# Kernel tuning notes

Measured on AMD Instinct MI355X. Metric: run time of the kernel, lower is better.

Reference implementation:

```python
import jax, jax.numpy as jnp
import numpy as np
from jax import lax

DN = ('NCHW', 'OIHW', 'NCHW')

def conv2d(x, w, b, stride, pad):
    y = lax.conv_general_dilated(x, w, (stride, stride), [(pad, pad), (pad, pad)], dimension_numbers=DN)
    return y + b[None, :, None, None]

def conv_transpose2d(x, w, b):
    # torch ConvTranspose2d(k=4, s=2, p=1): weight is (in, out, kH, kW).
    # Equivalent dilated conv: flip spatial dims, swap in/out, lhs_dilation=2, pad=k-1-p=2.
    kernel = jnp.flip(w, (2, 3)).transpose(1, 0, 2, 3)  # (out, in, 4, 4)
    y = lax.conv_general_dilated(x, kernel, (1, 1), [(2, 2), (2, 2)], lhs_dilation=(2, 2), dimension_numbers=DN)
    return y + b[None, :, None, None]

def res_block(x, w, b):
    return x + jax.nn.relu(conv2d(x, w, b, 1, 1))

def setup_inputs() -> dict:
    key = jax.random.key(0)
    ks = jax.random.split(key, 20)
    F_, K, D = 16, 64, 16  # num_features, num_embeddings, embedding_dim
    s = 0.05
    inp = {
        'x': jax.random.normal(ks[0], (64, 1, 256, 256), jnp.float32),
        'conv1_w': jax.random.normal(ks[1], (F_, 1, 4, 4), jnp.float32) * s,
        'conv1_b': jnp.zeros((F_,), jnp.float32),
        'conv2_w': jax.random.normal(ks[2], (F_, F_, 4, 4), jnp.float32) * s,
        'conv2_b': jnp.zeros((F_,), jnp.float32),
        'er1_w': jax.random.normal(ks[3], (F_, F_, 3, 3), jnp.float32) * s,
        'er1_b': jnp.zeros((F_,), jnp.float32),
        'er2_w': jax.random.normal(ks[4], (F_, F_, 3, 3), jnp.float32) * s,
        'er2_b': jnp.zeros((F_,), jnp.float32),
        'codebook': jax.random.normal(ks[5], (K, D), jnp.float32),
        'dr1_w': jax.random.normal(ks[6], (F_, F_, 3, 3), jnp.float32) * s,
        'dr1_b': jnp.zeros((F_,), jnp.float32),
        'dr2_w': jax.random.normal(ks[7], (F_, F_, 3, 3), jnp.float32) * s,
        'dr2_b': jnp.zeros((F_,), jnp.float32),
        'tc1_w': jax.random.normal(ks[8], (F_, F_, 4, 4), jnp.float32) * s,  # ConvTranspose (in,out,kH,kW)
        'tc1_b': jnp.zeros((F_,), jnp.float32),
        'tc2_w': jax.random.normal(ks[9], (F_, 1, 4, 4), jnp.float32) * s,
        'tc2_b': jnp.zeros((1,), jnp.float32),
    }
    return inp

def reference(x, conv1_w, conv1_b, conv2_w, conv2_b, er1_w, er1_b, er2_w, er2_b,
              codebook, dr1_w, dr1_b, dr2_w, dr2_b, tc1_w, tc1_b, tc2_w, tc2_b):
    # Encoder
    h = jax.nn.relu(conv2d(x, conv1_w, conv1_b, 2, 1))
    h = jax.nn.relu(conv2d(h, conv2_w, conv2_b, 2, 1))
    h = res_block(h, er1_w, er1_b)
    h = res_block(h, er2_w, er2_b)  # (B, 16, 64, 64)
    # VQ: faithful to torch's encoded.view(-1, C) raw NCHW flatten
    C = h.shape[1]
    flat = h.reshape(-1, C)  # (N, 16)
    # squared L2 distances without materializing (N, K, D) broadcast tensor
    d = (jnp.sum(flat * flat, axis=1, keepdims=True)
         - 2.0 * flat @ codebook.T
         + jnp.sum(codebook * codebook, axis=1)[None, :])  # (N, K)
    indices = jnp.argmin(d, axis=1)  # (N,)
    quantized = codebook[indices].reshape(h.shape)
    # Decoder
    q = res_block(quantized, dr1_w, dr1_b)
    q = res_block(q, dr2_w, dr2_b)
    q = jax.nn.relu(conv_transpose2d(q, tc1_w, tc1_b))
    decoded = conv_transpose2d(q, tc2_w, tc2_b)  # (B, 1, 256, 256)
    return decoded, indices
```

## Files before the change

### kernel.cpp

```cpp
#include <hip/hip_runtime.h>
#include <hip/hip_bf16.h>


#define R8X(M)  M(0) M(1) M(2) M(3) M(4) M(5) M(6) M(7)

typedef __attribute__((ext_vector_type(8))) short          bf16x8;
typedef __attribute__((ext_vector_type(8))) unsigned short u16x8;
typedef __attribute__((ext_vector_type(4))) float          f32x4;

__device__ __forceinline__ unsigned short f2bf(float f) {
    unsigned u; __builtin_memcpy(&u, &f, 4);
    unsigned r = u + 0x7FFFu + ((u >> 16) & 1u);
    return (unsigned short)(r >> 16);
}
__device__ __forceinline__ float bf2f(unsigned short h) {
    unsigned u = ((unsigned)h) << 16;
    float f; __builtin_memcpy(&f, &u, 4);
    return f;
}

__global__ __launch_bounds__(256) void conv1_k(const float* __restrict__ x, const float* __restrict__ w,
                                               const float* __restrict__ bias,
                                               unsigned short* __restrict__ oh, unsigned short* __restrict__ ol) {
    int idx = blockIdx.x * 256 + threadIdx.x;
    int ox = idx & 127;
    int oy = (idx >> 7) & 127;
    int b  = idx >> 14;
    const float* xin = x + (size_t)b * 65536;
    float pv[16];
#pragma unroll
    for (int ky = 0; ky < 4; ++ky) {
        int iy = 2 * oy - 1 + ky;
#pragma unroll
        for (int kx = 0; kx < 4; ++kx) {
            int ix = 2 * ox - 1 + kx;
            pv[ky * 4 + kx] = (iy >= 0 && iy < 256 && ix >= 0 && ix < 256)
                                  ? xin[iy * 256 + ix] : 0.f;
        }
    }
    u16x8 h0, h1, l0, l1;
#pragma unroll
    for (int oc = 0; oc < 16; ++oc) {
        float acc = bias[oc];
#pragma unroll
        for (int k = 0; k < 16; ++k) acc = fmaf(pv[k], w[oc * 16 + k], acc);
        float r = fmaxf(acc, 0.f);
        unsigned short hb = f2bf(r);
        unsigned short lb = f2bf(r - bf2f(hb));
        if (oc < 8) { h0[oc] = hb; l0[oc] = lb; }
        else        { h1[oc - 8] = hb; l1[oc - 8] = lb; }
    }
    u16x8* po = (u16x8*)(oh + (size_t)idx * 16);
    po[0] = h0; po[1] = h1;
    u16x8* pl = (u16x8*)(ol + (size_t)idx * 16);
    pl[0] = l0; pl[1] = l1;
}

__global__ __launch_bounds__(256) void conv2_mfma_k(const unsigned short* __restrict__ fh,
                                                    const unsigned short* __restrict__ fl,
                                                    const float* __restrict__ w, const float* __restrict__ bias,
                                                    float* __restrict__ out) {
    __shared__ unsigned short wsh[16 * 264];
    __shared__ unsigned short wsl[16 * 264];
    for (int i = threadIdx.x; i < 4096; i += 256) {
        int oc = i >> 8, k = i & 255;
        int ic = k & 15, tap = k >> 4;
        float f = w[oc * 256 + ic * 16 + tap];
        unsigned short hb = f2bf(f);
        wsh[oc * 264 + k] = hb;
        wsl[oc * 264 + k] = f2bf(f - bf2f(hb));
    }
    __syncthreads();

    int wid  = threadIdx.x >> 6;
    int lane = threadIdx.x & 63;
    int col = lane & 15;
    int kg  = lane >> 4;
    int ic0 = (kg & 1) * 8;
    float accb = bias[col];
    int gw = blockIdx.x * 4 + wid;

    for (int t = 0; t < 2; ++t) {
        int tile = gw * 2 + t;
        int v0  = (tile & 3) * 16;
        int y   = (tile >> 2) & 63;
        int img = tile >> 8;
        const unsigned short* bh = fh + (size_t)img * 262144;
        const unsigned short* bl = fl + (size_t)img * 262144;
        f32x4 acc = { accb, accb, accb, accb };
#pragma unroll
        for (int m = 0; m < 8; ++m) {
            int tap = 2 * m + (kg >> 1);
            int ty = tap >> 2, tx = tap & 3;
            int jy = 2 * y - 1 + ty;
            int jx = 2 * (v0 + col) - 1 + tx;
            bf16x8 ah = { 0, 0, 0, 0, 0, 0, 0, 0 };
            bf16x8 al = { 0, 0, 0, 0, 0, 0, 0, 0 };
            if (jy >= 0 && jy < 128 && jx >= 0 && jx < 128) {
                size_t off = ((size_t)(jy * 128 + jx)) * 16 + ic0;
                ah = *(const bf16x8*)(bh + off);
                al = *(const bf16x8*)(bl + off);
            }
            bf16x8 wh = *(const bf16x8*)&wsh[col * 264 + m * 32 + kg * 8];
            bf16x8 wl = *(const bf16x8*)&wsl[col * 264 + m * 32 + kg * 8];
            acc = __builtin_amdgcn_mfma_f32_16x16x32_bf16(ah, wh, acc, 0, 0, 0);
            acc = __builtin_amdgcn_mfma_f32_16x16x32_bf16(al, wh, acc, 0, 0, 0);
            acc = __builtin_amdgcn_mfma_f32_16x16x32_bf16(ah, wl, acc, 0, 0, 0);
        }
        float* o = out + (size_t)img * 65536 + col * 4096 + y * 64 + v0;
#pragma unroll
        for (int r = 0; r < 4; ++r) {
            int px = kg * 4 + r;
            o[px] = fmaxf(acc[r], 0.f);
        }
    }
}

__global__ __launch_bounds__(256) void res_k(const float* __restrict__ in, const float* __restrict__ w,
                                             const float* __restrict__ bias, float* __restrict__ out) {
    int half = blockIdx.x >> 10;
    int idx  = (blockIdx.x & 1023) * 256 + threadIdx.x;
    int ox = idx & 63;
    int oy = (idx >> 6) & 63;
    int b  = idx >> 12;
    int ocb = half * 8;
    const float* xin = in + (size_t)b * 65536;
    const float* wb  = w + (size_t)ocb * 144;
#define DECLB(i) float a##i = bias[ocb + i];
    R8X(DECLB)
#undef DECLB
    bool yt = (oy > 0), yb = (oy < 63);
    bool xl = (ox > 0), xr = (ox < 63);
    for (int ic = 0; ic < 16; ++ic) {
        const float* xb = xin + ic * 4096 + (oy - 1) * 64 + (ox - 1);
        float pa0 = (yt && xl) ? xb[0]       : 0.f;
        float pa1 =  yt        ? xb[1]       : 0.f;
        float pa2 = (yt && xr) ? xb[2]       : 0.f;
        float pb0 =  xl        ? xb[64 + 0]  : 0.f;
        float pb1 =              xb[64 + 1];
        float pb2 =  xr        ? xb[64 + 2]  : 0.f;
        float pc0 = (yb && xl) ? xb[128 + 0] : 0.f;
        float pc1 =  yb        ? xb[128 + 1] : 0.f;
        float pc2 = (yb && xr) ? xb[128 + 2] : 0.f;
        const float* wp = wb + ic * 9;
#define FMAR(oc) { const float* q = wp + oc * 144; \
        a##oc = fmaf(pa0, q[0], a##oc); a##oc = fmaf(pa1, q[1], a##oc); a##oc = fmaf(pa2, q[2], a##oc); \
        a##oc = fmaf(pb0, q[3], a##oc); a##oc = fmaf(pb1, q[4], a##oc); a##oc = fmaf(pb2, q[5], a##oc); \
        a##oc = fmaf(pc0, q[6], a##oc); a##oc = fmaf(pc1, q[7], a##oc); a##oc = fmaf(pc2, q[8], a##oc); }
        R8X(FMAR)
#undef FMAR
    }
    float* o        = out + (size_t)b * 65536 + (size_t)ocb * 4096 + oy * 64 + ox;
    const float* rr = xin + (size_t)ocb * 4096 + oy * 64 + ox;
#define RSTO(oc) o[oc * 4096] = rr[oc * 4096] + fmaxf(a##oc, 0.f);
    R8X(RSTO)
#undef RSTO
}

__global__ __launch_bounds__(256) void vq_k(const float* __restrict__ h, const float* __restrict__ cb,
                                            unsigned short* __restrict__ q, float* __restrict__ idx_out) {
    __shared__ float cbs[1024];
    __shared__ float cn[64];
    for (int i = threadIdx.x; i < 1024; i += 256) cbs[i] = cb[i];
    __syncthreads();
    if (threadIdx.x < 64) {
        float s = 0.f;
#pragma unroll
        for (int d = 0; d < 16; ++d) { float v = cbs[threadIdx.x * 16 + d]; s = fmaf(v, v, s); }
        cn[threadIdx.x] = s;
    }
    __syncthreads();
    int r = blockIdx.x * 256 + threadIdx.x;
    float f[16];
    const float4* hp = (const float4*)(h + (size_t)r * 16);
#pragma unroll
    for (int j = 0; j < 4; ++j) {
        float4 v = hp[j];
        f[j * 4 + 0] = v.x; f[j * 4 + 1] = v.y; f[j * 4 + 2] = v.z; f[j * 4 + 3] = v.w;
    }
    float best = 3.4e38f;
    int bi = 0;
    for (int k = 0; k < 64; ++k) {
        float dot = 0.f;
#pragma unroll
        for (int d = 0; d < 16; ++d) dot = fmaf(f[d], cbs[k * 16 + d], dot);
        float dist = cn[k] - 2.f * dot;
        if (dist < best) { best = dist; bi = k; }
    }
    u16x8 q0, q1;
#pragma unroll
    for (int d = 0; d < 8; ++d) {
        q0[d] = f2bf(cbs[bi * 16 + d]);
        q1[d] = f2bf(cbs[bi * 16 + 8 + d]);
    }
    u16x8* qp = (u16x8*)(q + (size_t)r * 16);
    qp[0] = q0; qp[1] = q1;
    idx_out[r] = (float)bi;
}

__global__ __launch_bounds__(256) void trans_k(const unsigned short* __restrict__ in,
                                               unsigned short* __restrict__ out) {
    __shared__ unsigned short lds[16 * 64];
    int b = blockIdx.x >> 6;
    int y = blockIdx.x & 63;
    int t = threadIdx.x;
    {
        int c = t >> 4, x0 = (t & 15) * 4;
        const unsigned short* p = in + (((size_t)(b * 16 + c) * 64 + y) << 6) + x0;
#pragma unroll
        for (int j = 0; j < 4; ++j) lds[c * 64 + x0 + j] = p[j];
    }
    __syncthreads();
    {
        int xx = t >> 2, c0 = (t & 3) * 4;
        unsigned short* p = out + (((size_t)(b * 64 + y) * 64 + xx) << 4) + c0;
#pragma unroll
        for (int j = 0; j < 4; ++j) p[j] = lds[(c0 + j) * 64 + xx];
    }
}

__global__ __launch_bounds__(256) void res_mfma_k(const unsigned short* __restrict__ in,
                                                  const float* __restrict__ w, const float* __restrict__ bias,
                                                  unsigned short* __restrict__ outb) {
    int wid  = threadIdx.x >> 6;
    int lane = threadIdx.x & 63;
    int col = lane & 15;
    int kg  = lane >> 4;
    int ic0 = (kg & 1) * 8;

    bf16x8 bw[5];
#pragma unroll
    for (int m = 0; m < 5; ++m) {
        int tap = 2 * m + (kg >> 1);
        bf16x8 t = { 0, 0, 0, 0, 0, 0, 0, 0 };
        if (tap < 9) {
#pragma unroll
            for (int j = 0; j < 8; ++j)
                t[j] = (short)f2bf(w[(col * 16 + ic0 + j) * 9 + tap]);
        }
        bw[m] = t;
    }
    float accb = bias[col];

    int gw = blockIdx.x * 4 + wid;
    for (int t = 0; t < 8; ++t) {
        int tile = gw * 8 + t;
        int v0  = (tile & 3) * 16;
        int y   = (tile >> 2) & 63;
        int img = tile >> 8;
        const unsigned short* xi = in + (size_t)img * 65536;
        f32x4 acc = { accb, accb, accb, accb };
#pragma unroll
        for (int m = 0; m < 5; ++m) {
            int tap = 2 * m + (kg >> 1);
            bf16x8 a = { 0, 0, 0, 0, 0, 0, 0, 0 };
            if (tap < 9) {
                int ty = tap / 3, tx = tap - ty * 3;
                int jy = y + ty - 1;
                int jx = v0 + col + tx - 1;
                if (jy >= 0 && jy < 64 && jx >= 0 && jx < 64)
                    a = *(const bf16x8*)(xi + ((jy * 64 + jx) * 16 + ic0));
            }
            acc = __builtin_amdgcn_mfma_f32_16x16x32_bf16(a, bw[m], acc, 0, 0, 0);
        }
#pragma unroll
        for (int r = 0; r < 4; ++r) {
            int px = v0 + kg * 4 + r;
            size_t ad = (size_t)(y * 64 + px) * 16 + col;
            float vin = bf2f(xi[ad]);
            outb[(size_t)img * 65536 + ad] = f2bf(vin + fmaxf(acc[r], 0.f));
        }
    }
}

__global__ __launch_bounds__(256) void tconv1_mfma_k(const unsigned short* __restrict__ xb,
                                                     const float* __restrict__ w1, const float* __restrict__ bia,
                                                     unsigned short* __restrict__ outb) {
    int cls = blockIdx.x >> 9;
    int bb  = blockIdx.x & 511;
    int DY = cls >> 1, DX = cls & 1;
    int wid  = threadIdx.x >> 6;
    int lane = threadIdx.x & 63;
    int oc = lane & 15;
    int kg = lane >> 4;

    bf16x8 bfr0, bfr1;
    float accb = bia[oc];
#pragma unroll
    for (int m = 0; m < 2; ++m) {
        int tap = 2 * m + (kg >> 1);
        int ty = tap >> 1, tx = tap & 1;
        int koff = (3 - DY - 2 * ty) * 4 + (3 - DX - 2 * tx);
        int ic0 = (kg & 1) * 8;
        bf16x8 t;
#pragma unroll
        for (int j = 0; j < 8; ++j)
            t[j] = (short)f2bf(w1[(ic0 + j) * 256 + oc * 16 + koff]);
        if (m == 0) bfr0 = t; else bfr1 = t;
    }

    int Wc = bb * 4 + wid;
    for (int t = 0; t < 8; ++t) {
        int tile = Wc * 8 + t;
        int v0  = (tile & 3) * 16;
        int u   = (tile >> 2) & 63;
        int img = tile >> 8;
        const unsigned short* xi = xb + (size_t)img * 65536;
        f32x4 acc = { accb, accb, accb, accb };
#pragma unroll
        for (int m = 0; m < 2; ++m) {
            int tap = 2 * m + (kg >> 1);
            int ty = tap >> 1, tx = tap & 1;
            int jy = u + DY - 1 + ty;
            int jx = v0 + oc + DX - 1 + tx;
            bf16x8 a = { 0, 0, 0, 0, 0, 0, 0, 0 };
            if (jy >= 0 && jy < 64 && jx >= 0 && jx < 64) {
                int ic0 = (kg & 1) * 8;
                a = *(const bf16x8*)(xi + ((jy * 64 + jx) * 16 + ic0));
            }
            acc = __builtin_amdgcn_mfma_f32_16x16x32_bf16(a, (m == 0 ? bfr0 : bfr1), acc, 0, 0, 0);
        }
        int my = 2 * u + DY;
#pragma unroll
        for (int r = 0; r < 4; ++r) {
            int pxr = kg * 4 + r;
            int mx  = 2 * (v0 + pxr) + DX;
            outb[(((size_t)img * 16384) + my * 128 + mx) * 16 + oc] = f2bf(fmaxf(acc[r], 0.f));
        }
    }
}

template <int RY, int RX>
__device__ __forceinline__ void quad_contrib(const unsigned short* __restrict__ px,
                                             const float* __restrict__ w2,
                                             float& a00, float& a01, float& a10, float& a11) {
    constexpr int nY = (RY == 0) ? 2 : 1;
    constexpr int nX = (RX == 0) ? 2 : 1;
    constexpr int dyA[2] = { (RY == 1) ? 1 : 0, 1 };
    constexpr int kyA[2] = { (RY == -1) ? 3 : ((RY == 0) ? 1 : 0), 2 };
    constexpr int dxA[2] = { (RX == 1) ? 1 : 0, 1 };
    constexpr int kxA[2] = { (RX == -1) ? 3 : ((RX == 0) ? 1 : 0), 2 };
    u16x8 h0 = *(const u16x8*)px;
    u16x8 h1 = *(const u16x8*)(px + 8);
#pragma unroll
    for (int iy = 0; iy < nY; ++iy) {
#pragma unroll
        for (int ix = 0; ix < nX; ++ix) {
            const int ky = kyA[iy], kx = kxA[ix];
            float& a = (dyA[iy] == 0) ? ((dxA[ix] == 0) ? a00 : a01)
                                      : ((dxA[ix] == 0) ? a10 : a11);
#pragma unroll
            for (int ic = 0; ic < 8; ++ic)
                a = fmaf(bf2f(h0[ic]), w2[ic * 16 + ky * 4 + kx], a);
#pragma unroll
            for (int ic = 0; ic < 8; ++ic)
                a = fmaf(bf2f(h1[ic]), w2[(ic + 8) * 16 + ky * 4 + kx], a);
        }
    }
}

__global__ __launch_bounds__(256) void tconv2_quad_k(const unsigned short* __restrict__ f1b,
                                                     const float* __restrict__ w2, const float* __restrict__ b2,
                                                     float* __restrict__ out) {
    int idx = blockIdx.x * 256 + threadIdx.x;
    int v = idx & 127;
    int u = (idx >> 7) & 127;
    int b = idx >> 14;
    const unsigned short* fb = f1b + (size_t)b * 262144;
    float b2s = b2[0];
    float a00 = b2s, a01 = b2s, a10 = b2s, a11 = b2s;

#define QC(RY, RX) { int jy = u + (RY), jx = v + (RX); \
    if (jy >= 0 && jy < 128 && jx >= 0 && jx < 128) \
        quad_contrib<RY, RX>(fb + ((size_t)(jy * 128 + jx) << 4), w2, a00, a01, a10, a11); }
    QC(-1, -1) QC(-1, 0) QC(-1, 1)
    QC( 0, -1) QC( 0, 0) QC( 0, 1)
    QC( 1, -1) QC( 1, 0) QC( 1, 1)
#undef QC

    float* o = out + (size_t)b * 65536 + (2 * u) * 256 + 2 * v;
    float2 r0; r0.x = a00; r0.y = a01;
    float2 r1; r1.x = a10; r1.y = a11;
    *(float2*)o         = r0;
    *(float2*)(o + 256) = r1;
}

extern "C" void kernel_launch(void* const* d_in, const int* in_sizes, int n_in,
                              void* d_out, int out_size, void* d_ws, size_t ws_size,
                              hipStream_t stream) {
    const float* x    = (const float*)d_in[0];
    const float* c1w  = (const float*)d_in[1];
    const float* c1b  = (const float*)d_in[2];
    const float* c2w  = (const float*)d_in[3];
    const float* c2b  = (const float*)d_in[4];
    const float* er1w = (const float*)d_in[5];
    const float* er1b = (const float*)d_in[6];
    const float* er2w = (const float*)d_in[7];
    const float* er2b = (const float*)d_in[8];
    const float* cb   = (const float*)d_in[9];
    const float* dr1w = (const float*)d_in[10];
    const float* dr1b = (const float*)d_in[11];
    const float* dr2w = (const float*)d_in[12];
    const float* dr2b = (const float*)d_in[13];
    const float* t1w  = (const float*)d_in[14];
    const float* t1b  = (const float*)d_in[15];
    const float* t2w  = (const float*)d_in[16];
    const float* t2b  = (const float*)d_in[17];

    char* W = (char*)d_ws;
    const size_t MB = 1024 * 1024;
    unsigned short* f1h   = (unsigned short*)(W + 0);
    unsigned short* f1l   = (unsigned short*)(W + 32 * MB);
    float*          f2c   = (float*)         (W + 64 * MB);
    float*          fer1  = (float*)         (W + 80 * MB);
    float*          fer2  = (float*)         (W + 96 * MB);
    unsigned short* qn    = (unsigned short*)(W + 112 * MB);
    unsigned short* qc    = (unsigned short*)(W + 128 * MB);
    unsigned short* d1o   = (unsigned short*)(W + 144 * MB);
    unsigned short* d2o   = (unsigned short*)(W + 160 * MB);
    unsigned short* t1o   = (unsigned short*)(W + 176 * MB);

    float* out     = (float*)d_out;
    float* idx_out = out + 4194304;

    conv1_k      <<<4096, 256, 0, stream>>>(x, c1w, c1b, f1h, f1l);
    conv2_mfma_k <<<2048, 256, 0, stream>>>(f1h, f1l, c2w, c2b, f2c);
    res_k        <<<2048, 256, 0, stream>>>(f2c, er1w, er1b, fer1);
    res_k        <<<2048, 256, 0, stream>>>(fer1, er2w, er2b, fer2);
    vq_k         <<<1024, 256, 0, stream>>>(fer2, cb, qn, idx_out);
    trans_k      <<<4096, 256, 0, stream>>>(qn, qc);
    res_mfma_k   <<< 512, 256, 0, stream>>>(qc, dr1w, dr1b, d1o);
    res_mfma_k   <<< 512, 256, 0, stream>>>(d1o, dr2w, dr2b, d2o);
    tconv1_mfma_k<<<2048, 256, 0, stream>>>(d2o, t1w, t1b, t1o);
    tconv2_quad_k<<<4096, 256, 0, stream>>>(t1o, t2w, t2b, out);
}
```

Before: 223.4 us.

## Move encoder residual convs to split-bf16 MFMA with NHWC hi/lo activations

Replaces the scalar FP32 encoder residual-block kernel with an MFMA kernel that uses a split-bf16 (hi+lo) three-product scheme to keep near-FP32 accuracy. conv2 now writes its output as NHWC hi/lo bf16 pairs, so the first residual block reads them directly and writes hi/lo again. The second block writes NCHW float for the VQ stage. This cuts the scalar FMA work and the float memory traffic of the two encoder res blocks, at the cost of less scattered-store efficiency and some bf16 split precision.

```diff
diff --git a/kernel.cpp b/kernel.cpp
--- a/kernel.cpp
+++ b/kernel.cpp
@@ -59,7 +59,7 @@
 __global__ __launch_bounds__(256) void conv2_mfma_k(const unsigned short* __restrict__ fh,
                                                     const unsigned short* __restrict__ fl,
                                                     const float* __restrict__ w, const float* __restrict__ bias,
-                                                    float* __restrict__ out) {
+                                                    unsigned short* __restrict__ oh, unsigned short* __restrict__ ol) {
     __shared__ unsigned short wsh[16 * 264];
     __shared__ unsigned short wsl[16 * 264];
     for (int i = threadIdx.x; i < 4096; i += 256) {
@@ -107,54 +107,87 @@
             acc = __builtin_amdgcn_mfma_f32_16x16x32_bf16(al, wh, acc, 0, 0, 0);
             acc = __builtin_amdgcn_mfma_f32_16x16x32_bf16(ah, wl, acc, 0, 0, 0);
         }
-        float* o = out + (size_t)img * 65536 + col * 4096 + y * 64 + v0;
 #pragma unroll
         for (int r = 0; r < 4; ++r) {
-            int px = kg * 4 + r;
-            o[px] = fmaxf(acc[r], 0.f);
-        }
-    }
-}
-
-__global__ __launch_bounds__(256) void res_k(const float* __restrict__ in, const float* __restrict__ w,
-                                             const float* __restrict__ bias, float* __restrict__ out) {
-    int half = blockIdx.x >> 10;
-    int idx  = (blockIdx.x & 1023) * 256 + threadIdx.x;
-    int ox = idx & 63;
-    int oy = (idx >> 6) & 63;
-    int b  = idx >> 12;
-    int ocb = half * 8;
-    const float* xin = in + (size_t)b * 65536;
-    const float* wb  = w + (size_t)ocb * 144;
-#define DECLB(i) float a##i = bias[ocb + i];
-    R8X(DECLB)
-#undef DECLB
-    bool yt = (oy > 0), yb = (oy < 63);
-    bool xl = (ox > 0), xr = (ox < 63);
-    for (int ic = 0; ic < 16; ++ic) {
-        const float* xb = xin + ic * 4096 + (oy - 1) * 64 + (ox - 1);
-        float pa0 = (yt && xl) ? xb[0]       : 0.f;
-        float pa1 =  yt        ? xb[1]       : 0.f;
-        float pa2 = (yt && xr) ? xb[2]       : 0.f;
-        float pb0 =  xl        ? xb[64 + 0]  : 0.f;
-        float pb1 =              xb[64 + 1];
-        float pb2 =  xr        ? xb[64 + 2]  : 0.f;
-        float pc0 = (yb && xl) ? xb[128 + 0] : 0.f;
-        float pc1 =  yb        ? xb[128 + 1] : 0.f;
-        float pc2 = (yb && xr) ? xb[128 + 2] : 0.f;
-        const float* wp = wb + ic * 9;
-#define FMAR(oc) { const float* q = wp + oc * 144; \
-        a##oc = fmaf(pa0, q[0], a##oc); a##oc = fmaf(pa1, q[1], a##oc); a##oc = fmaf(pa2, q[2], a##oc); \
-        a##oc = fmaf(pb0, q[3], a##oc); a##oc = fmaf(pb1, q[4], a##oc); a##oc = fmaf(pb2, q[5], a##oc); \
-        a##oc = fmaf(pc0, q[6], a##oc); a##oc = fmaf(pc1, q[7], a##oc); a##oc = fmaf(pc2, q[8], a##oc); }
-        R8X(FMAR)
-#undef FMAR
-    }
-    float* o        = out + (size_t)b * 65536 + (size_t)ocb * 4096 + oy * 64 + ox;
-    const float* rr = xin + (size_t)ocb * 4096 + oy * 64 + ox;
-#define RSTO(oc) o[oc * 4096] = rr[oc * 4096] + fmaxf(a##oc, 0.f);
-    R8X(RSTO)
-#undef RSTO
+            int xx = v0 + kg * 4 + r;
+            size_t ad = (size_t)img * 65536 + ((size_t)(y * 64 + xx)) * 16 + col;
+            float rv = fmaxf(acc[r], 0.f);
+            unsigned short hb = f2bf(rv);
+            oh[ad] = hb;
+            ol[ad] = f2bf(rv - bf2f(hb));
+        }
+    }
+}
+
+template <int OUTMODE>
+__global__ __launch_bounds__(256) void er_mfma_k(const unsigned short* __restrict__ inh,
+                                                 const unsigned short* __restrict__ inl,
+                                                 const float* __restrict__ w, const float* __restrict__ bias,
+                                                 unsigned short* __restrict__ oh, unsigned short* __restrict__ ol,
+                                                 float* __restrict__ ofp) {
+    __shared__ unsigned short wsh[16 * 176];
+    __shared__ unsigned short wsl[16 * 176];
+    for (int i = threadIdx.x; i < 2816; i += 256) {
+        int oc = i / 176, k = i % 176;
+        float f = (k < 144) ? w[(oc * 16 + (k & 15)) * 9 + (k >> 4)] : 0.f;
+        unsigned short hb = f2bf(f);
+        wsh[i] = hb;
+        wsl[i] = f2bf(f - bf2f(hb));
+    }
+    __syncthreads();
+
+    int wid  = threadIdx.x >> 6;
+    int lane = threadIdx.x & 63;
+    int col = lane & 15;
+    int kg  = lane >> 4;
+    int ic0 = (kg & 1) * 8;
+    float accb = bias[col];
+    int gw = blockIdx.x * 4 + wid;
+
+    for (int t = 0; t < 8; ++t) {
+        int tile = gw * 8 + t;
+        int v0  = (tile & 3) * 16;
+        int y   = (tile >> 2) & 63;
+        int img = tile >> 8;
+        const unsigned short* xh = inh + (size_t)img * 65536;
+        const unsigned short* xl = inl + (size_t)img * 65536;
+        f32x4 acc = { accb, accb, accb, accb };
+#pragma unroll
+        for (int m = 0; m < 5; ++m) {
+            int tap = 2 * m + (kg >> 1);
+            bf16x8 ah = { 0, 0, 0, 0, 0, 0, 0, 0 };
+            bf16x8 al = { 0, 0, 0, 0, 0, 0, 0, 0 };
+            if (tap < 9) {
+                int ty = tap / 3, tx = tap - ty * 3;
+                int jy = y + ty - 1;
+                int jx = v0 + col + tx - 1;
+                if (jy >= 0 && jy < 64 && jx >= 0 && jx < 64) {
+                    size_t off = ((size_t)(jy * 64 + jx)) * 16 + ic0;
+                    ah = *(const bf16x8*)(xh + off);
+                    al = *(const bf16x8*)(xl + off);
+                }
+            }
+            bf16x8 wh = *(const bf16x8*)&wsh[col * 176 + m * 32 + kg * 8];
+            bf16x8 wl = *(const bf16x8*)&wsl[col * 176 + m * 32 + kg * 8];
+            acc = __builtin_amdgcn_mfma_f32_16x16x32_bf16(ah, wh, acc, 0, 0, 0);
+            acc = __builtin_amdgcn_mfma_f32_16x16x32_bf16(al, wh, acc, 0, 0, 0);
+            acc = __builtin_amdgcn_mfma_f32_16x16x32_bf16(ah, wl, acc, 0, 0, 0);
+        }
+#pragma unroll
+        for (int r = 0; r < 4; ++r) {
+            int px = v0 + kg * 4 + r;
+            size_t ad = ((size_t)(y * 64 + px)) * 16 + col;
+            float vin = bf2f(xh[ad]) + bf2f(xl[ad]);
+            float res = vin + fmaxf(acc[r], 0.f);
+            if (OUTMODE == 0) {
+                unsigned short hb = f2bf(res);
+                oh[(size_t)img * 65536 + ad] = hb;
+                ol[(size_t)img * 65536 + ad] = f2bf(res - bf2f(hb));
+            } else {
+                ofp[(size_t)img * 65536 + (size_t)col * 4096 + y * 64 + px] = res;
+            }
+        }
+    }
 }
 
 __global__ __launch_bounds__(256) void vq_k(const float* __restrict__ h, const float* __restrict__ cb,
@@ -409,25 +442,27 @@
 
     char* W = (char*)d_ws;
     const size_t MB = 1024 * 1024;
-    unsigned short* f1h   = (unsigned short*)(W + 0);
-    unsigned short* f1l   = (unsigned short*)(W + 32 * MB);
-    float*          f2c   = (float*)         (W + 64 * MB);
-    float*          fer1  = (float*)         (W + 80 * MB);
-    float*          fer2  = (float*)         (W + 96 * MB);
-    unsigned short* qn    = (unsigned short*)(W + 112 * MB);
-    unsigned short* qc    = (unsigned short*)(W + 128 * MB);
-    unsigned short* d1o   = (unsigned short*)(W + 144 * MB);
-    unsigned short* d2o   = (unsigned short*)(W + 160 * MB);
-    unsigned short* t1o   = (unsigned short*)(W + 176 * MB);
+    unsigned short* f1h = (unsigned short*)(W + 0);
+    unsigned short* f1l = (unsigned short*)(W + 32 * MB);
+    unsigned short* c2h = (unsigned short*)(W + 64 * MB);
+    unsigned short* c2l = (unsigned short*)(W + 80 * MB);
+    unsigned short* e1h = (unsigned short*)(W + 96 * MB);
+    unsigned short* e1l = (unsigned short*)(W + 112 * MB);
+    float*          e2f = (float*)         (W + 128 * MB);
+    unsigned short* qn  = (unsigned short*)(W + 152 * MB);
+    unsigned short* qc  = (unsigned short*)(W + 168 * MB);
+    unsigned short* d1o = (unsigned short*)(W + 184 * MB);
+    unsigned short* d2o = (unsigned short*)(W + 200 * MB);
+    unsigned short* t1o = (unsigned short*)(W + 216 * MB);
 
     float* out     = (float*)d_out;
     float* idx_out = out + 4194304;
 
     conv1_k      <<<4096, 256, 0, stream>>>(x, c1w, c1b, f1h, f1l);
-    conv2_mfma_k <<<2048, 256, 0, stream>>>(f1h, f1l, c2w, c2b, f2c);
-    res_k        <<<2048, 256, 0, stream>>>(f2c, er1w, er1b, fer1);
-    res_k        <<<2048, 256, 0, stream>>>(fer1, er2w, er2b, fer2);
-    vq_k         <<<1024, 256, 0, stream>>>(fer2, cb, qn, idx_out);
+    conv2_mfma_k <<<2048, 256, 0, stream>>>(f1h, f1l, c2w, c2b, c2h, c2l);
+    er_mfma_k<0> <<< 512, 256, 0, stream>>>(c2h, c2l, er1w, er1b, e1h, e1l, nullptr);
+    er_mfma_k<1> <<< 512, 256, 0, stream>>>(e1h, e1l, er2w, er2b, nullptr, nullptr, e2f);
+    vq_k         <<<1024, 256, 0, stream>>>(e2f, cb, qn, idx_out);
     trans_k      <<<4096, 256, 0, stream>>>(qn, qc);
     res_mfma_k   <<< 512, 256, 0, stream>>>(qc, dr1w, dr1b, d1o);
     res_mfma_k   <<< 512, 256, 0, stream>>>(d1o, dr2w, dr2b, d2o);
```

Result: faster. 214.1 us (-4.2%).
